# Performance work log

Hardware: AMD Instinct MI355X
Metric: run time of the kernel (lower is better)

The kernel has to match this reference:

```python
import jax, jax.numpy as jnp
import numpy as np

N, E = 100000, 600000
DIN, DEMB, DOUT = 128, 128, 2
EPS = 1e-5


def setup_inputs() -> dict:
    key = jax.random.key(0)
    ks = jax.random.split(key, 20)
    s = 1.0 / np.sqrt(DIN)
    se = 1.0 / np.sqrt(DEMB)
    inp = {
        'x': jax.random.normal(ks[0], (N, DIN), jnp.float32),
        'edge_index': jax.random.randint(ks[1], (2, E), 0, N, jnp.int64),
        # SAGEConv layer 0 (in->emb): lin_l (with bias) on aggregated, lin_r (no bias) on root
        'Wl0': jax.random.uniform(ks[2], (DIN, DEMB), jnp.float32, -s, s),
        'bl0': jax.random.uniform(ks[3], (DEMB,), jnp.float32, -s, s),
        'Wr0': jax.random.uniform(ks[4], (DIN, DEMB), jnp.float32, -s, s),
        # SAGEConv layer 1 (emb->emb)
        'Wl1': jax.random.uniform(ks[5], (DEMB, DEMB), jnp.float32, -se, se),
        'bl1': jax.random.uniform(ks[6], (DEMB,), jnp.float32, -se, se),
        'Wr1': jax.random.uniform(ks[7], (DEMB, DEMB), jnp.float32, -se, se),
        # BatchNorm affine params (2 BN layers used)
        'g0': jnp.ones((DEMB,), jnp.float32),
        'be0': jnp.zeros((DEMB,), jnp.float32),
        'g1': jnp.ones((DEMB,), jnp.float32),
        'be1': jnp.zeros((DEMB,), jnp.float32),
        # MLP head
        'W1': jax.random.uniform(ks[8], (DEMB, DEMB), jnp.float32, -se, se),
        'b1': jax.random.uniform(ks[9], (DEMB,), jnp.float32, -se, se),
        'W2': jax.random.uniform(ks[10], (DEMB, DEMB), jnp.float32, -se, se),
        'b2': jax.random.uniform(ks[11], (DEMB,), jnp.float32, -se, se),
        'W3': jax.random.uniform(ks[12], (DEMB, DOUT), jnp.float32, -se, se),
        'b3': jax.random.uniform(ks[13], (DOUT,), jnp.float32, -se, se),
    }
    return inp


def _sage_conv(x, edge_index, Wl, bl, Wr):
    # sum-aggregate source features into destination nodes, then transform
    src, dst = edge_index[0], edge_index[1]
    agg = jax.ops.segment_sum(x[src], dst, num_segments=x.shape[0])  # [N, d]
    return agg @ Wl + bl + x @ Wr


def _bn_relu(h, gamma, beta):
    mu = jnp.mean(h, axis=0)
    var = jnp.var(h, axis=0)
    return jax.nn.relu((h - mu) * jax.lax.rsqrt(var + EPS) * gamma + beta)


def reference(x, edge_index, Wl0, bl0, Wr0, Wl1, bl1, Wr1,
              g0, be0, g1, be1, W1, b1, W2, b2, W3, b3):
    # NOTE: original forward zips num_layers convs with num_layers-1 batch_norms,
    # so only the first num_layers-1 = 2 conv blocks execute.
    h = _bn_relu(_sage_conv(x, edge_index, Wl0, bl0, Wr0), g0, be0)
    h = _bn_relu(_sage_conv(h, edge_index, Wl1, bl1, Wr1), g1, be1)
    # dropout p=0.2 is identity in inference mode
    h = jax.nn.relu(h @ W1 + b1)
    h = jax.nn.relu(h @ W2 + b2)
    return h @ W3 + b3
```

## Files before the change

### kernel.cpp

```cpp
#include <hip/hip_runtime.h>

#define EPS 1e-5f

typedef __attribute__((ext_vector_type(8))) short bf16x8;
typedef __attribute__((ext_vector_type(4))) float f32x4;

#define GLOBAL_LOAD_LDS16(gp, lp) \
    __builtin_amdgcn_global_load_lds((const __attribute__((address_space(1))) unsigned int*)(gp), \
                                     (__attribute__((address_space(3))) unsigned int*)(lp), 16, 0, 0)

static __device__ __forceinline__ void split8(float4 f0, float4 f1, bf16x8& hi, bf16x8& lo) {
    float f[8] = {f0.x, f0.y, f0.z, f0.w, f1.x, f1.y, f1.z, f1.w};
    bf16x8 h, l;
#pragma unroll
    for (int i = 0; i < 8; ++i) {
        unsigned u = __float_as_uint(f[i]);
        h[i] = (short)(u >> 16);
        float r = f[i] - __uint_as_float(u & 0xffff0000u);
        l[i] = (short)(__float_as_uint(r) >> 16);
    }
    hi = h; lo = l;
}

static __device__ __forceinline__ float4 bnrelu4(float4 v, float4 a, float4 d) {
    float4 r;
    r.x = fmaxf(a.x * v.x + d.x, 0.f);
    r.y = fmaxf(a.y * v.y + d.y, 0.f);
    r.z = fmaxf(a.z * v.z + d.z, 0.f);
    r.w = fmaxf(a.w * v.w + d.w, 0.f);
    return r;
}

__global__ __launch_bounds__(256) void hist_kernel(
    const int* __restrict__ ei, int* __restrict__ deg, int E)
{
    int e = blockIdx.x * 256 + threadIdx.x;
    if (e >= E) return;
    atomicAdd(&deg[ei[E + e]], 1);
}

__global__ __launch_bounds__(256) void blocksum_kernel(
    const int* __restrict__ deg, int* __restrict__ bsum, int N)
{
    int i = blockIdx.x * 256 + threadIdx.x;
    int v = (i < N) ? deg[i] : 0;
#pragma unroll
    for (int o = 1; o < 64; o <<= 1) v += __shfl_xor(v, o);
    __shared__ int s[4];
    if ((threadIdx.x & 63) == 0) s[threadIdx.x >> 6] = v;
    __syncthreads();
    if (threadIdx.x == 0) bsum[blockIdx.x] = s[0] + s[1] + s[2] + s[3];
}

__global__ __launch_bounds__(512) void scanb_kernel(int* bsum, int NB)
{
    __shared__ int sh[512];
    int t = threadIdx.x;
    int v = (t < NB) ? bsum[t] : 0;
    sh[t] = v;
    __syncthreads();
    for (int o = 1; o < 512; o <<= 1) {
        int add = (t >= o) ? sh[t - o] : 0;
        __syncthreads();
        sh[t] += add;
        __syncthreads();
    }
    if (t < NB) bsum[t] = (t == 0) ? 0 : sh[t - 1];
}

__global__ __launch_bounds__(256) void scanfinal_kernel(
    const int* __restrict__ deg, const int* __restrict__ bsum,
    int* __restrict__ rowptr, int* __restrict__ cursor, int N)
{
    int b = blockIdx.x, t = threadIdx.x;
    int i = b * 256 + t;
    int v = (i < N) ? deg[i] : 0;
    __shared__ int sh[256];
    sh[t] = v;
    __syncthreads();
    for (int o = 1; o < 256; o <<= 1) {
        int add = (t >= o) ? sh[t - o] : 0;
        __syncthreads();
        sh[t] += add;
        __syncthreads();
    }
    int excl = sh[t] - v;
    if (i < N) {
        int rp = bsum[b] + excl;
        rowptr[i] = rp;
        cursor[i] = rp;
        if (i == N - 1) rowptr[N] = rp + v;
    }
}

__global__ __launch_bounds__(256) void fill_kernel(
    const int* __restrict__ ei, int* __restrict__ cursor, int* __restrict__ col, int E)
{
    int e = blockIdx.x * 256 + threadIdx.x;
    if (e >= E) return;
    int d = ei[E + e];
    int pos = atomicAdd(&cursor[d], 1);
    col[pos] = ei[e];
}

template<int BN>
__global__ __launch_bounds__(256) void gather_kernel(
    const float* __restrict__ feat, float* __restrict__ agg,
    const int* __restrict__ rowptr, const int* __restrict__ colIdx,
    const float* __restrict__ bnst, int N)
{
    int gid = blockIdx.x * 256 + threadIdx.x;
    int n = gid >> 5;
    if (n >= N) return;
    int l = gid & 31;
    float4 a4, d4;
    if (BN) {
        a4 = *(const float4*)(bnst + 256 + l * 4);
        d4 = *(const float4*)(bnst + 384 + l * 4);
    }
    int beg = rowptr[n], end = rowptr[n + 1];
    float ax = 0.f, ay = 0.f, az = 0.f, aw = 0.f;
    float bx = 0.f, by = 0.f, bz = 0.f, bw = 0.f;
    int e = beg;
    for (; e + 2 <= end; e += 2) {
        int s0 = colIdx[e], s1 = colIdx[e + 1];
        float4 v0 = *(const float4*)(feat + (size_t)s0 * 128 + l * 4);
        float4 v1 = *(const float4*)(feat + (size_t)s1 * 128 + l * 4);
        if (BN) { v0 = bnrelu4(v0, a4, d4); v1 = bnrelu4(v1, a4, d4); }
        ax += v0.x; ay += v0.y; az += v0.z; aw += v0.w;
        bx += v1.x; by += v1.y; bz += v1.z; bw += v1.w;
    }
    if (e < end) {
        int s0 = colIdx[e];
        float4 v0 = *(const float4*)(feat + (size_t)s0 * 128 + l * 4);
        if (BN) v0 = bnrelu4(v0, a4, d4);
        ax += v0.x; ay += v0.y; az += v0.z; aw += v0.w;
    }
    *(float4*)(agg + (size_t)n * 128 + l * 4) =
        make_float4(ax + bx, ay + by, az + bz, aw + bw);
}

__global__ __launch_bounds__(256) void prepack_kernel(
    const float* __restrict__ W0, const float* __restrict__ W1,
    const float* __restrict__ W2, const float* __restrict__ W3,
    const float* __restrict__ W4, const float* __restrict__ W5,
    ushort* __restrict__ wPk)
{
    int m = blockIdx.y;
    const float* W = (m == 0) ? W0 : (m == 1) ? W1 : (m == 2) ? W2
                   : (m == 3) ? W3 : (m == 4) ? W4 : W5;
    int base = m * 32768;
#pragma unroll
    for (int t = 0; t < 8; ++t) {
        int idx = blockIdx.x * 2048 + t * 256 + threadIdx.x;
        int j = idx & 7, l = (idx >> 3) & 63, cf = (idx >> 9) & 7, kb = idx >> 12;
        int k = kb * 32 + (l >> 4) * 8 + j;
        int n = cf * 16 + (l & 15);
        float v = W[k * 128 + n];
        unsigned u = __float_as_uint(v);
        wPk[base + idx] = (ushort)(u >> 16);
        float r = v - __uint_as_float(u & 0xffff0000u);
        wPk[base + 16384 + idx] = (ushort)(__float_as_uint(r) >> 16);
    }
}

template<int DUAL, int RELU, int STATS, int BN>
__global__ __launch_bounds__(512, 2) void plin_kernel(
    const float* __restrict__ Xa, const float* __restrict__ Xb,
    const ushort* __restrict__ wPair, const float* __restrict__ bias,
    const float* __restrict__ bnst, float* __restrict__ Y,
    float* __restrict__ stOut, int nrows)
{
    extern __shared__ ushort lds[];
    ushort* ldsB = lds;
    float*  ldsA = (float*)(lds + (DUAL ? 65536 : 32768));
    const int tid  = threadIdx.x;
    const int lane = tid & 63;
    const int w    = tid >> 6;
    const int q = lane >> 4, s = lane & 15;

    {
        const int npass = DUAL ? 16 : 8;
#pragma unroll
        for (int p = 0; p < npass; ++p) {
            int cid = p * 8 + w;
            GLOBAL_LOAD_LDS16(wPair + (size_t)cid * 512 + lane * 8, ldsB + (size_t)cid * 512);
        }
    }

    const int srow  = tid >> 5;
    const int sunit = tid & 31;
    const int sux   = sunit ^ (srow & 7);
    float4 bna, bnd;
    if (BN) {
        bna = *(const float4*)(bnst + 256 + sunit * 4);
        bnd = *(const float4*)(bnst + 384 + sunit * 4);
    }

    const int colc = w * 16 + s;
    const float bv = bias[colc];
    float cs = 0.f, cq = 0.f;

    const int NT = (nrows + 15) >> 4;
    const int stride = (int)gridDim.x;
    const int t0 = blockIdx.x;

    if (t0 < NT) {
        int row = t0 * 16 + srow; if (row > nrows - 1) row = nrows - 1;
        float4 va = *(const float4*)(Xa + (size_t)row * 128 + sunit * 4);
        float4 vb;
        if (DUAL) vb = *(const float4*)(Xb + (size_t)row * 128 + sunit * 4);
        if (BN) { if (DUAL) vb = bnrelu4(vb, bna, bnd); else va = bnrelu4(va, bna, bnd); }
        *(float4*)(ldsA + srow * 128 + sux * 4) = va;
        if (DUAL) *(float4*)(ldsA + 2048 + srow * 128 + sux * 4) = vb;
    }

    for (int t = t0; t < NT; t += stride) {
        int tn = t + stride;
        float4 na, nb;
        if (tn < NT) {
            int row = tn * 16 + srow; if (row > nrows - 1) row = nrows - 1;
            na = *(const float4*)(Xa + (size_t)row * 128 + sunit * 4);
            if (DUAL) nb = *(const float4*)(Xb + (size_t)row * 128 + sunit * 4);
        }
        __syncthreads();

        f32x4 acc = (f32x4){0.f, 0.f, 0.f, 0.f};
#pragma unroll
        for (int m = 0; m <= DUAL; ++m) {
            const float*  ar = ldsA + m * 2048 + s * 128;
            const ushort* br = ldsB + m * 32768 + w * 512 + lane * 8;
#pragma unroll
            for (int kb = 0; kb < 4; ++kb) {
                int u0 = kb * 8 + q * 2;
                float4 f0 = *(const float4*)(ar + ((u0 + 0) ^ (s & 7)) * 4);
                float4 f1 = *(const float4*)(ar + ((u0 + 1) ^ (s & 7)) * 4);
                bf16x8 ah, al;
                split8(f0, f1, ah, al);
                bf16x8 bh = *(const bf16x8*)(br + kb * 4096);
                bf16x8 bl = *(const bf16x8*)(br + 16384 + kb * 4096);
                acc = __builtin_amdgcn_mfma_f32_16x16x32_bf16(ah, bh, acc, 0, 0, 0);
                acc = __builtin_amdgcn_mfma_f32_16x16x32_bf16(al, bh, acc, 0, 0, 0);
                acc = __builtin_amdgcn_mfma_f32_16x16x32_bf16(ah, bl, acc, 0, 0, 0);
            }
        }

        int r0 = t * 16 + q * 4;
#pragma unroll
        for (int i = 0; i < 4; ++i) {
            int r = r0 + i;
            if (r < nrows) {
                float y = acc[i] + bv;
                if (RELU) y = fmaxf(y, 0.f);
                Y[(size_t)r * 128 + colc] = y;
                if (STATS) { cs += y; cq += y * y; }
            }
        }
        __syncthreads();
        if (tn < NT) {
            if (BN) { if (DUAL) nb = bnrelu4(nb, bna, bnd); else na = bnrelu4(na, bna, bnd); }
            *(float4*)(ldsA + srow * 128 + sux * 4) = na;
            if (DUAL) *(float4*)(ldsA + 2048 + srow * 128 + sux * 4) = nb;
        }
    }

    if (STATS) {
        cs += __shfl_xor(cs, 16); cs += __shfl_xor(cs, 32);
        cq += __shfl_xor(cq, 16); cq += __shfl_xor(cq, 32);
        if (q == 0) {
            atomicAdd(&stOut[colc], cs);
            atomicAdd(&stOut[128 + colc], cq);
        }
    }
}

__global__ void finalize_kernel(float* st, const float* __restrict__ g,
                                const float* __restrict__ be, float inv_n)
{
    int c = threadIdx.x;
    float mu = st[c] * inv_n;
    float var = st[128 + c] * inv_n - mu * mu;
    float rs = rsqrtf(var + EPS);
    float a = g[c] * rs;
    st[256 + c] = a;
    st[384 + c] = be[c] - mu * a;
}

__global__ __launch_bounds__(256) void linout_kernel(
    const float* __restrict__ X, const float* __restrict__ W, const float* __restrict__ b,
    float* __restrict__ out, int nrows)
{
    int r = blockIdx.x * 256 + threadIdx.x;
    if (r >= nrows) return;
    float a0 = 0.f, a1 = 0.f;
    const float* xr = X + (size_t)r * 128;
#pragma unroll 8
    for (int k = 0; k < 128; k += 4) {
        float4 x = *(const float4*)(xr + k);
        a0 += x.x * W[(k + 0) * 2]     + x.y * W[(k + 1) * 2]
            + x.z * W[(k + 2) * 2]     + x.w * W[(k + 3) * 2];
        a1 += x.x * W[(k + 0) * 2 + 1] + x.y * W[(k + 1) * 2 + 1]
            + x.z * W[(k + 2) * 2 + 1] + x.w * W[(k + 3) * 2 + 1];
    }
    float2 o = make_float2(a0 + b[0], a1 + b[1]);
    *(float2*)(out + (size_t)r * 2) = o;
}

extern "C" void kernel_launch(void* const* d_in, const int* in_sizes, int n_in,
                              void* d_out, int out_size, void* d_ws, size_t ws_size,
                              hipStream_t stream) {
    const float* x   = (const float*)d_in[0];
    const int*   ei  = (const int*)d_in[1];
    const float* Wl0 = (const float*)d_in[2];
    const float* bl0 = (const float*)d_in[3];
    const float* Wr0 = (const float*)d_in[4];
    const float* Wl1 = (const float*)d_in[5];
    const float* bl1 = (const float*)d_in[6];
    const float* Wr1 = (const float*)d_in[7];
    const float* g0  = (const float*)d_in[8];
    const float* be0 = (const float*)d_in[9];
    const float* g1  = (const float*)d_in[10];
    const float* be1 = (const float*)d_in[11];
    const float* W1  = (const float*)d_in[12];
    const float* b1  = (const float*)d_in[13];
    const float* W2  = (const float*)d_in[14];
    const float* b2  = (const float*)d_in[15];
    const float* W3  = (const float*)d_in[16];
    const float* b3  = (const float*)d_in[17];
    float* out = (float*)d_out;

    const int N = in_sizes[0] / 128;
    const int E = in_sizes[1] / 2;

    float* A   = (float*)d_ws;
    float* B   = A + (size_t)N * 128;
    float* st0 = B + (size_t)N * 128;
    float* st1 = st0 + 512;
    ushort* wPk = (ushort*)(st1 + 512);
    int* deg    = (int*)(wPk + 6 * 32768);
    int* rowptr = deg + N;
    int* cursor = rowptr + N + 1;
    int* col    = cursor + N;
    int* bsum   = col + E;

    const int edgeGrid   = (E + 255) / 256;
    const int nodeGrid   = (N + 255) / 256;
    const int gatherGrid = ((size_t)N * 32 + 255) / 256;
    const float inv_n = 1.0f / (float)N;
    const size_t shDual = 147456;
    const size_t shSing = 73728;

    prepack_kernel<<<dim3(8, 6), 256, 0, stream>>>(Wl0, Wr0, Wl1, Wr1, W1, W2, wPk);

    hipMemsetAsync(deg, 0, (size_t)N * sizeof(int), stream);
    hist_kernel<<<edgeGrid, 256, 0, stream>>>(ei, deg, E);
    blocksum_kernel<<<nodeGrid, 256, 0, stream>>>(deg, bsum, N);
    scanb_kernel<<<1, 512, 0, stream>>>(bsum, nodeGrid);
    scanfinal_kernel<<<nodeGrid, 256, 0, stream>>>(deg, bsum, rowptr, cursor, N);
    fill_kernel<<<edgeGrid, 256, 0, stream>>>(ei, cursor, col, E);

    gather_kernel<0><<<gatherGrid, 256, 0, stream>>>(x, A, rowptr, col, nullptr, N);
    hipMemsetAsync(st0, 0, 256 * sizeof(float), stream);
    plin_kernel<1, 0, 1, 0><<<256, 512, shDual, stream>>>(
        A, x, wPk, bl0, nullptr, A, st0, N);
    finalize_kernel<<<1, 128, 0, stream>>>(st0, g0, be0, inv_n);

    gather_kernel<1><<<gatherGrid, 256, 0, stream>>>(A, B, rowptr, col, st0, N);
    hipMemsetAsync(st1, 0, 256 * sizeof(float), stream);
    plin_kernel<1, 0, 1, 1><<<256, 512, shDual, stream>>>(
        B, A, wPk + 2 * 32768, bl1, st0, B, st1, N);
    finalize_kernel<<<1, 128, 0, stream>>>(st1, g1, be1, inv_n);

    plin_kernel<0, 1, 0, 1><<<512, 512, shSing, stream>>>(
        B, nullptr, wPk + 4 * 32768, b1, st1, A, nullptr, N);
    plin_kernel<0, 1, 0, 0><<<512, 512, shSing, stream>>>(
        A, nullptr, wPk + 5 * 32768, b2, nullptr, B, nullptr, N);
    linout_kernel<<<(N + 255) / 256, 256, 0, stream>>>(B, W3, b3, out, N);
}
```

Before: 334.9 us.

## Keep weights in registers and pre-split activations to bf16 in padded LDS

Weight fragments now load straight into registers per wave instead of being staged through a large dynamic LDS buffer. Activations are split into bf16 hi/lo once when written to LDS, using a padded row stride in place of the XOR swizzle, so the inner loop reads ready-made bf16x8 fragments. This shrinks LDS use, so the dual kernels now launch 512 blocks instead of 256, and the split work is done once per element rather than in every wave. The cost is higher register pressure (up to 16 bf16x8 weight fragments held per thread), which may hurt occupancy under the (512,2) launch bound.

```diff
diff --git a/kernel.cpp b/kernel.cpp
--- a/kernel.cpp
+++ b/kernel.cpp
@@ -5,21 +5,18 @@
 typedef __attribute__((ext_vector_type(8))) short bf16x8;
 typedef __attribute__((ext_vector_type(4))) float f32x4;
 
-#define GLOBAL_LOAD_LDS16(gp, lp) \
-    __builtin_amdgcn_global_load_lds((const __attribute__((address_space(1))) unsigned int*)(gp), \
-                                     (__attribute__((address_space(3))) unsigned int*)(lp), 16, 0, 0)
-
-static __device__ __forceinline__ void split8(float4 f0, float4 f1, bf16x8& hi, bf16x8& lo) {
-    float f[8] = {f0.x, f0.y, f0.z, f0.w, f1.x, f1.y, f1.z, f1.w};
-    bf16x8 h, l;
-#pragma unroll
-    for (int i = 0; i < 8; ++i) {
-        unsigned u = __float_as_uint(f[i]);
-        h[i] = (short)(u >> 16);
-        float r = f[i] - __uint_as_float(u & 0xffff0000u);
-        l[i] = (short)(__float_as_uint(r) >> 16);
-    }
-    hi = h; lo = l;
+static __device__ __forceinline__ void split4(float4 f, ushort4& hi, ushort4& lo) {
+    float v[4] = {f.x, f.y, f.z, f.w};
+    ushort h[4], l[4];
+#pragma unroll
+    for (int i = 0; i < 4; ++i) {
+        unsigned u = __float_as_uint(v[i]);
+        h[i] = (ushort)(u >> 16);
+        float r = v[i] - __uint_as_float(u & 0xffff0000u);
+        l[i] = (ushort)(__float_as_uint(r) >> 16);
+    }
+    hi = make_ushort4(h[0], h[1], h[2], h[3]);
+    lo = make_ushort4(l[0], l[1], l[2], l[3]);
 }
 
 static __device__ __forceinline__ float4 bnrelu4(float4 v, float4 a, float4 d) {
@@ -171,26 +168,25 @@
     const float* __restrict__ bnst, float* __restrict__ Y,
     float* __restrict__ stOut, int nrows)
 {
-    extern __shared__ ushort lds[];
-    ushort* ldsB = lds;
-    float*  ldsA = (float*)(lds + (DUAL ? 65536 : 32768));
+    __shared__ ushort ldsA[(DUAL ? 2 : 1) * 2 * 2176];
     const int tid  = threadIdx.x;
     const int lane = tid & 63;
     const int w    = tid >> 6;
     const int q = lane >> 4, s = lane & 15;
 
-    {
-        const int npass = DUAL ? 16 : 8;
-#pragma unroll
-        for (int p = 0; p < npass; ++p) {
-            int cid = p * 8 + w;
-            GLOBAL_LOAD_LDS16(wPair + (size_t)cid * 512 + lane * 8, ldsB + (size_t)cid * 512);
-        }
-    }
+    constexpr int NM = DUAL + 1;
+    bf16x8 wf[NM][4][2];
+#pragma unroll
+    for (int m = 0; m < NM; ++m)
+#pragma unroll
+        for (int kb = 0; kb < 4; ++kb) {
+            size_t o = (size_t)m * 32768 + (size_t)kb * 4096 + w * 512 + lane * 8;
+            wf[m][kb][0] = *(const bf16x8*)(wPair + o);
+            wf[m][kb][1] = *(const bf16x8*)(wPair + o + 16384);
+        }
 
     const int srow  = tid >> 5;
     const int sunit = tid & 31;
-    const int sux   = sunit ^ (srow & 7);
     float4 bna, bnd;
     if (BN) {
         bna = *(const float4*)(bnst + 256 + sunit * 4);
@@ -204,6 +200,7 @@
     const int NT = (nrows + 15) >> 4;
     const int stride = (int)gridDim.x;
     const int t0 = blockIdx.x;
+    const int woff = srow * 136 + sunit * 4;
 
     if (t0 < NT) {
         int row = t0 * 16 + srow; if (row > nrows - 1) row = nrows - 1;
@@ -211,8 +208,15 @@
         float4 vb;
         if (DUAL) vb = *(const float4*)(Xb + (size_t)row * 128 + sunit * 4);
         if (BN) { if (DUAL) vb = bnrelu4(vb, bna, bnd); else va = bnrelu4(va, bna, bnd); }
-        *(float4*)(ldsA + srow * 128 + sux * 4) = va;
-        if (DUAL) *(float4*)(ldsA + 2048 + srow * 128 + sux * 4) = vb;
+        ushort4 h, l;
+        split4(va, h, l);
+        *(ushort4*)(ldsA + woff)        = h;
+        *(ushort4*)(ldsA + 2176 + woff) = l;
+        if (DUAL) {
+            split4(vb, h, l);
+            *(ushort4*)(ldsA + 4352 + woff) = h;
+            *(ushort4*)(ldsA + 6528 + woff) = l;
+        }
     }
 
     for (int t = t0; t < NT; t += stride) {
@@ -227,21 +231,15 @@
 
         f32x4 acc = (f32x4){0.f, 0.f, 0.f, 0.f};
 #pragma unroll
-        for (int m = 0; m <= DUAL; ++m) {
-            const float*  ar = ldsA + m * 2048 + s * 128;
-            const ushort* br = ldsB + m * 32768 + w * 512 + lane * 8;
+        for (int m = 0; m < NM; ++m) {
+            const ushort* pm = ldsA + m * 4352 + s * 136;
 #pragma unroll
             for (int kb = 0; kb < 4; ++kb) {
-                int u0 = kb * 8 + q * 2;
-                float4 f0 = *(const float4*)(ar + ((u0 + 0) ^ (s & 7)) * 4);
-                float4 f1 = *(const float4*)(ar + ((u0 + 1) ^ (s & 7)) * 4);
-                bf16x8 ah, al;
-                split8(f0, f1, ah, al);
-                bf16x8 bh = *(const bf16x8*)(br + kb * 4096);
-                bf16x8 bl = *(const bf16x8*)(br + 16384 + kb * 4096);
-                acc = __builtin_amdgcn_mfma_f32_16x16x32_bf16(ah, bh, acc, 0, 0, 0);
-                acc = __builtin_amdgcn_mfma_f32_16x16x32_bf16(al, bh, acc, 0, 0, 0);
-                acc = __builtin_amdgcn_mfma_f32_16x16x32_bf16(ah, bl, acc, 0, 0, 0);
+                bf16x8 ah = *(const bf16x8*)(pm + (kb * 4 + q) * 8);
+                bf16x8 al = *(const bf16x8*)(pm + 2176 + (kb * 4 + q) * 8);
+                acc = __builtin_amdgcn_mfma_f32_16x16x32_bf16(ah, wf[m][kb][0], acc, 0, 0, 0);
+                acc = __builtin_amdgcn_mfma_f32_16x16x32_bf16(al, wf[m][kb][0], acc, 0, 0, 0);
+                acc = __builtin_amdgcn_mfma_f32_16x16x32_bf16(ah, wf[m][kb][1], acc, 0, 0, 0);
             }
         }
 
@@ -259,8 +257,15 @@
         __syncthreads();
         if (tn < NT) {
             if (BN) { if (DUAL) nb = bnrelu4(nb, bna, bnd); else na = bnrelu4(na, bna, bnd); }
-            *(float4*)(ldsA + srow * 128 + sux * 4) = na;
-            if (DUAL) *(float4*)(ldsA + 2048 + srow * 128 + sux * 4) = nb;
+            ushort4 h, l;
+            split4(na, h, l);
+            *(ushort4*)(ldsA + woff)        = h;
+            *(ushort4*)(ldsA + 2176 + woff) = l;
+            if (DUAL) {
+                split4(nb, h, l);
+                *(ushort4*)(ldsA + 4352 + woff) = h;
+                *(ushort4*)(ldsA + 6528 + woff) = l;
+            }
         }
     }
 
@@ -347,8 +352,6 @@
     const int nodeGrid   = (N + 255) / 256;
     const int gatherGrid = ((size_t)N * 32 + 255) / 256;
     const float inv_n = 1.0f / (float)N;
-    const size_t shDual = 147456;
-    const size_t shSing = 73728;
 
     prepack_kernel<<<dim3(8, 6), 256, 0, stream>>>(Wl0, Wr0, Wl1, Wr1, W1, W2, wPk);
 
@@ -361,19 +364,19 @@
 
     gather_kernel<0><<<gatherGrid, 256, 0, stream>>>(x, A, rowptr, col, nullptr, N);
     hipMemsetAsync(st0, 0, 256 * sizeof(float), stream);
-    plin_kernel<1, 0, 1, 0><<<256, 512, shDual, stream>>>(
+    plin_kernel<1, 0, 1, 0><<<512, 512, 0, stream>>>(
         A, x, wPk, bl0, nullptr, A, st0, N);
     finalize_kernel<<<1, 128, 0, stream>>>(st0, g0, be0, inv_n);
 
     gather_kernel<1><<<gatherGrid, 256, 0, stream>>>(A, B, rowptr, col, st0, N);
     hipMemsetAsync(st1, 0, 256 * sizeof(float), stream);
-    plin_kernel<1, 0, 1, 1><<<256, 512, shDual, stream>>>(
+    plin_kernel<1, 0, 1, 1><<<512, 512, 0, stream>>>(
         B, A, wPk + 2 * 32768, bl1, st0, B, st1, N);
     finalize_kernel<<<1, 128, 0, stream>>>(st1, g1, be1, inv_n);
 
-    plin_kernel<0, 1, 0, 1><<<512, 512, shSing, stream>>>(
+    plin_kernel<0, 1, 0, 1><<<512, 512, 0, stream>>>(
         B, nullptr, wPk + 4 * 32768, b1, st1, A, nullptr, N);
-    plin_kernel<0, 1, 0, 0><<<512, 512, shSing, stream>>>(
+    plin_kernel<0, 1, 0, 0><<<512, 512, 0, stream>>>(
         A, nullptr, wPk + 5 * 32768, b2, nullptr, B, nullptr, N);
     linout_kernel<<<(N + 255) / 256, 256, 0, stream>>>(B, W3, b3, out, N);
 }
```

Result: faster. 299.3 us (-10.6%).
